# Optimization experiments

Measured on AMD Instinct MI355X. Metric: run time of the kernel, lower is better.

The kernel has to match this reference:

```python
import jax, jax.numpy as jnp
import numpy as np

NEG = -9e15  # sentinel used by the torch module for masked logits


def setup_inputs() -> dict:
    key = jax.random.key(0)
    k_x, k_nl, k_q, k_k, k_v = jax.random.split(key, 5)
    n, m, nhid = 50000, 16, 128
    x = jax.random.normal(k_x, (n, nhid), dtype=jnp.float32)
    neighbor_list = jax.random.randint(k_nl, (n, m), 0, n)  # value n-1 == padding
    # xavier_uniform with gain=1.414 for square (nhid, nhid) matrices
    bound = 1.414 * np.sqrt(6.0 / (nhid + nhid))
    Q = jax.random.uniform(k_q, (nhid, nhid), jnp.float32, -bound, bound)
    K = jax.random.uniform(k_k, (nhid, nhid), jnp.float32, -bound, bound)
    V = jax.random.uniform(k_v, (nhid, nhid), jnp.float32, -bound, bound)
    return {"x": x, "neighbor_list": neighbor_list, "Q": Q, "K": K, "V": V}


def _forward(x, neighbor_list, Q, K, V):
    n, nhid = x.shape
    scare = jnp.asarray(nhid ** 0.5, x.dtype)
    # masks: neighbor index n-1 means padding
    mask = (neighbor_list != n - 1).astype(x.dtype)            # (n, m)
    mask1 = mask[:, :, None] * mask[:, None, :]                # (n, m, m)
    mask2 = jnp.concatenate([jnp.ones((n, 1), x.dtype), mask], axis=1)[:, None, :]  # (n,1,m+1)

    # ---- stage 1: neighbor-level attention ----
    nm = x[neighbor_list]                                      # (n, m, h) gather
    Qn = jnp.einsum('nmk,kh->nmh', nm, Q)
    Kn = jnp.einsum('nmk,kh->nmh', nm, K)
    Vn = jnp.einsum('nmk,kh->nmh', nm, V)
    s = jnp.einsum('nih,njh->nij', Qn, Kn)                     # (n, m, m)
    s = jax.nn.leaky_relu(s, 0.01)
    s = jnp.where(mask1 > 0, s, NEG) * scare                   # faithful: scale after mask
    a = jax.nn.softmax(s, axis=2)                              # dropout is identity (eval)
    nres = jnp.einsum('nij,njh->nih', a, Vn)                   # (n, m, h)

    # ---- stage 2: node-level attention over [self, neighbors] ----
    xr = x[:, None, :]                                         # (n, 1, h)
    cat = jnp.concatenate([xr, nres], axis=1)                  # (n, m+1, h)
    Qx = jnp.einsum('nik,kh->nih', xr, Q)                      # (n, 1, h)
    Kc = jnp.einsum('njk,kh->njh', cat, K)
    Vc = jnp.einsum('njk,kh->njh', cat, V)
    s2 = jnp.einsum('nih,njh->nij', Qx, Kc) * scare            # (n, 1, m+1)
    s2 = jax.nn.leaky_relu(s2, 0.01)
    s2 = jnp.where(mask2 > 0, s2, NEG)
    a2 = jax.nn.softmax(s2, axis=2)
    out = jnp.einsum('nij,njh->nih', a2, Vc)[:, 0, :]          # (n, h)

    # F.normalize: L2 along dim 1, eps 1e-12
    norm = jnp.linalg.norm(out, axis=1, keepdims=True)
    return out / jnp.maximum(norm, 1e-12)


def reference(x, neighbor_list, Q, K, V):
    return _forward(x, neighbor_list, Q, K, V)
```

## Files before the change

### kernel.cpp

```cpp
#include <hip/hip_runtime.h>
#include <math.h>

#define NEG_CONST (-9000000000000000.0f)
#define SCARE 11.313708498984761f

#define DPP_XOR1  0xB1
#define DPP_XOR2  0x4E
#define DPP_XOR7  0x141
#define DPP_XOR15 0x140

template<int CTRL>
__device__ __forceinline__ float dpp_add(float x) {
    int yi = __builtin_amdgcn_update_dpp(0, __float_as_int(x), CTRL, 0xF, 0xF, true);
    return x + __int_as_float(yi);
}
template<int CTRL>
__device__ __forceinline__ float dpp_max(float x) {
    int yi = __builtin_amdgcn_update_dpp(0, __float_as_int(x), CTRL, 0xF, 0xF, true);
    return fmaxf(x, __int_as_float(yi));
}

__device__ __forceinline__ void wave_lds_fence() {
    __builtin_amdgcn_wave_barrier();
    asm volatile("s_waitcnt lgkmcnt(0)" ::: "memory");
    __builtin_amdgcn_wave_barrier();
}
__device__ __forceinline__ void wave_vm_fence() {
    __builtin_amdgcn_wave_barrier();
    asm volatile("s_waitcnt vmcnt(0) lgkmcnt(0)" ::: "memory");
    __builtin_amdgcn_wave_barrier();
}

__global__ __launch_bounds__(256) void small_mm_a(const float* __restrict__ Q,
                                                  const float* __restrict__ K,
                                                  const float* __restrict__ V,
                                                  float* __restrict__ QKt,
                                                  float* __restrict__ VV) {
    int r  = blockIdx.x * 8 + (threadIdx.x >> 5);
    int c0 = (threadIdx.x & 31) * 4;
    float a0 = 0.f, a1 = 0.f, a2 = 0.f, a3 = 0.f;
    if (blockIdx.y == 0) {
        for (int k = 0; k < 128; k += 4) {
            float4 q  = *reinterpret_cast<const float4*>(&Q[r * 128 + k]);
            float4 k0 = *reinterpret_cast<const float4*>(&K[(c0 + 0) * 128 + k]);
            float4 k1 = *reinterpret_cast<const float4*>(&K[(c0 + 1) * 128 + k]);
            float4 k2 = *reinterpret_cast<const float4*>(&K[(c0 + 2) * 128 + k]);
            float4 k3 = *reinterpret_cast<const float4*>(&K[(c0 + 3) * 128 + k]);
            a0 += q.x*k0.x + q.y*k0.y + q.z*k0.z + q.w*k0.w;
            a1 += q.x*k1.x + q.y*k1.y + q.z*k1.z + q.w*k1.w;
            a2 += q.x*k2.x + q.y*k2.y + q.z*k2.z + q.w*k2.w;
            a3 += q.x*k3.x + q.y*k3.y + q.z*k3.z + q.w*k3.w;
        }
        float4 o = {a0, a1, a2, a3};
        *reinterpret_cast<float4*>(&QKt[r * 128 + c0]) = o;
    } else {
        for (int k = 0; k < 128; ++k) {
            float a = V[r * 128 + k];
            float4 b = *reinterpret_cast<const float4*>(&V[k * 128 + c0]);
            a0 += a * b.x; a1 += a * b.y; a2 += a * b.z; a3 += a * b.w;
        }
        float4 o = {a0, a1, a2, a3};
        *reinterpret_cast<float4*>(&VV[r * 128 + c0]) = o;
    }
}

__global__ __launch_bounds__(256) void small_mm_b(const float* __restrict__ QKt,
                                                  const float* __restrict__ V,
                                                  float* __restrict__ MT) {
    int r  = blockIdx.x * 8 + (threadIdx.x >> 5);
    int c0 = (threadIdx.x & 31) * 4;
    float a0 = 0.f, a1 = 0.f, a2 = 0.f, a3 = 0.f;
    for (int k = 0; k < 128; k += 4) {
        float4 q  = *reinterpret_cast<const float4*>(&QKt[r * 128 + k]);
        float4 k0 = *reinterpret_cast<const float4*>(&V[(c0 + 0) * 128 + k]);
        float4 k1 = *reinterpret_cast<const float4*>(&V[(c0 + 1) * 128 + k]);
        float4 k2 = *reinterpret_cast<const float4*>(&V[(c0 + 2) * 128 + k]);
        float4 k3 = *reinterpret_cast<const float4*>(&V[(c0 + 3) * 128 + k]);
        a0 += q.x*k0.x + q.y*k0.y + q.z*k0.z + q.w*k0.w;
        a1 += q.x*k1.x + q.y*k1.y + q.z*k1.z + q.w*k1.w;
        a2 += q.x*k2.x + q.y*k2.y + q.z*k2.z + q.w*k2.w;
        a3 += q.x*k3.x + q.y*k3.y + q.z*k3.z + q.w*k3.w;
    }
    float4 o = {a0, a1, a2, a3};
    *reinterpret_cast<float4*>(&MT[r * 128 + c0]) = o;
}

__global__ __launch_bounds__(256) void proj_gemm(
    const float* __restrict__ x,
    const float* __restrict__ W0, const float* __restrict__ W1,
    const float* __restrict__ W2,
    float* __restrict__ G, float* __restrict__ O1, float* __restrict__ O2,
    int n)
{
    __shared__ __align__(16) float xs[32][132];
    __shared__ __align__(16) float ws[32][132];

    const float* Wsel[3] = {W0, W1, W2};
    float*       Osel[3] = {G, O1, O2};
    const int    osr[3]  = {256, 128, 128};
    const int    oof[3]  = {128, 0, 0};
    int yb = blockIdx.y;
    const float* W = Wsel[yb];
    float*       O = Osel[yb];
    int ostride = osr[yb];
    int ooff = oof[yb];
    int row0 = blockIdx.x * 128;
    int tid = threadIdx.x;
    int tr = tid >> 4, tc = tid & 15;

    float acc[8][8] = {};
    for (int kk = 0; kk < 128; kk += 32) {
        #pragma unroll
        for (int it = 0; it < 4; ++it) {
            int id = tid + it * 256;
            int r = id >> 3;
            int f = id & 7;
            int grow = row0 + r;
            float4 v = (grow < n)
                ? *reinterpret_cast<const float4*>(&x[(size_t)grow * 128 + kk + f * 4])
                : make_float4(0.f, 0.f, 0.f, 0.f);
            xs[f * 4 + 0][r] = v.x; xs[f * 4 + 1][r] = v.y;
            xs[f * 4 + 2][r] = v.z; xs[f * 4 + 3][r] = v.w;
            if (yb == 0 && grow < n)
                *reinterpret_cast<float4*>(&G[(size_t)grow * 256 + kk + f * 4]) = v;
        }
        #pragma unroll
        for (int it = 0; it < 4; ++it) {
            int id = tid + it * 256;
            int k = id >> 5;
            int c4 = id & 31;
            *reinterpret_cast<float4*>(&ws[k][c4 * 4]) =
                *reinterpret_cast<const float4*>(&W[(size_t)(kk + k) * 128 + c4 * 4]);
        }
        __syncthreads();
        #pragma unroll 4
        for (int k = 0; k < 32; ++k) {
            float4 a0 = *reinterpret_cast<const float4*>(&xs[k][tr * 8]);
            float4 a1 = *reinterpret_cast<const float4*>(&xs[k][tr * 8 + 4]);
            float4 b0 = *reinterpret_cast<const float4*>(&ws[k][tc * 8]);
            float4 b1 = *reinterpret_cast<const float4*>(&ws[k][tc * 8 + 4]);
            float av[8] = {a0.x, a0.y, a0.z, a0.w, a1.x, a1.y, a1.z, a1.w};
            float bv[8] = {b0.x, b0.y, b0.z, b0.w, b1.x, b1.y, b1.z, b1.w};
            #pragma unroll
            for (int i2 = 0; i2 < 8; ++i2)
                #pragma unroll
                for (int j2 = 0; j2 < 8; ++j2)
                    acc[i2][j2] += av[i2] * bv[j2];
        }
        __syncthreads();
    }
    #pragma unroll
    for (int i2 = 0; i2 < 8; ++i2) {
        int grow = row0 + tr * 8 + i2;
        if (grow < n) {
            float4 o0 = {acc[i2][0], acc[i2][1], acc[i2][2], acc[i2][3]};
            float4 o1 = {acc[i2][4], acc[i2][5], acc[i2][6], acc[i2][7]};
            *reinterpret_cast<float4*>(&O[(size_t)grow * ostride + ooff + tc * 8])     = o0;
            *reinterpret_cast<float4*>(&O[(size_t)grow * ostride + ooff + tc * 8 + 4]) = o1;
        }
    }
}

__global__ __launch_bounds__(64, 5) void node_attn(
    const int* __restrict__ nlist,
    const float* __restrict__ G,
    float* uy,
    float* __restrict__ c0a,
    int n)
{
    __shared__ __align__(16) float Bs[2048];
    __shared__ __align__(16) float Ts[16];

    const int l  = threadIdx.x;
    const int g  = l >> 2;
    const int jj = l & 3;
    const int i  = blockIdx.x;

    int nlv = 0;
    if (l < 16) nlv = nlist[(size_t)i * 16 + l];
    unsigned long long mb = __ballot(l < 16 ? (nlv != n - 1) : 0);

    {
        int sub   = l & 31;
        int sigma = ((sub & 3) << 3) | (sub >> 2);
        int half  = l >> 5;
        #pragma unroll
        for (int p = 0; p < 8; ++p) {
            int nr = __shfl(nlv, 2 * p + half, 64);
            const float* src = &G[(size_t)nr * 256 + sigma * 4];
            __builtin_amdgcn_global_load_lds(
                (const __attribute__((address_space(1))) unsigned int*)src,
                (__attribute__((address_space(3))) unsigned int*)&Bs[p * 256],
                16, 0, 0);
        }
    }

    float2 qa = *reinterpret_cast<const float2*>(&G[(size_t)i * 256 + 128 + l * 2]);
    float2 xa = *reinterpret_cast<const float2*>(&G[(size_t)i * 256 + l * 2]);
    float s200 = qa.x * xa.x + qa.y * xa.y;
    s200 = dpp_add<DPP_XOR1>(s200);
    s200 = dpp_add<DPP_XOR2>(s200);
    s200 = dpp_add<DPP_XOR7>(s200);
    s200 = dpp_add<DPP_XOR15>(s200);
    s200 += __shfl_xor(s200, 16, 64);
    s200 += __shfl_xor(s200, 32, 64);

    int nl_g = __shfl(nlv, g, 64);
    float4 A[8];
    {
        const float* ab = &G[(size_t)nl_g * 256 + 128 + jj * 32];
        #pragma unroll
        for (int k4 = 0; k4 < 8; ++k4)
            A[k4] = *reinterpret_cast<const float4*>(&ab[k4 * 4]);
    }

    wave_vm_fence();

    float a[16];
    {
        float sc[16];
        #pragma unroll
        for (int c = 0; c < 16; ++c) {
            const float* bb = &Bs[c * 128 + jj * 4];
            float acc = 0.f;
            #pragma unroll
            for (int k4 = 0; k4 < 8; ++k4) {
                float4 b = *reinterpret_cast<const float4*>(&bb[k4 * 16]);
                acc += A[k4].x * b.x + A[k4].y * b.y + A[k4].z * b.z + A[k4].w * b.w;
            }
            acc = dpp_add<DPP_XOR1>(acc);
            acc = dpp_add<DPP_XOR2>(acc);
            sc[c] = acc;
        }
        bool rlive = (mb >> g) & 1ULL;
        float m = -3.0e38f;
        #pragma unroll
        for (int c = 0; c < 16; ++c) {
            float s = sc[c];
            float slr = s > 0.f ? s : 0.01f * s;
            bool live = rlive && ((mb >> c) & 1ULL);
            float sm = (live ? slr : NEG_CONST) * SCARE;
            sc[c] = sm;
            m = fmaxf(m, sm);
        }
        float ssum = 0.f;
        #pragma unroll
        for (int c = 0; c < 16; ++c) { float p = __expf(sc[c] - m); a[c] = p; ssum += p; }
        float rs = 1.f / ssum;
        #pragma unroll
        for (int c = 0; c < 16; ++c) a[c] *= rs;
    }

    {
        float acc = 0.f;
        #pragma unroll
        for (int k4 = 0; k4 < 8; ++k4) {
            int kx = (k4 + g) & 7;
            float4 b  = *reinterpret_cast<const float4*>(&Bs[g * 128 + kx * 16 + jj * 4]);
            float4 uu = *reinterpret_cast<const float4*>(&uy[(size_t)i * 128 + jj * 32 + kx * 4]);
            acc += uu.x * b.x + uu.y * b.y + uu.z * b.z + uu.w * b.w;
        }
        acc = dpp_add<DPP_XOR1>(acc);
        acc = dpp_add<DPP_XOR2>(acc);
        if (jj == 0) Ts[g] = acc;
    }
    wave_lds_fence();
    float tarr[16];
    {
        #pragma unroll
        for (int q4 = 0; q4 < 4; ++q4) {
            float4 t4 = *reinterpret_cast<const float4*>(&Ts[q4 * 4]);
            tarr[q4 * 4 + 0] = t4.x; tarr[q4 * 4 + 1] = t4.y;
            tarr[q4 * 4 + 2] = t4.z; tarr[q4 * 4 + 3] = t4.w;
        }
    }

    float lg = 0.f;
    #pragma unroll
    for (int k = 0; k < 16; ++k) lg += a[k] * tarr[k];
    {
        float v = lg * SCARE;
        v = v > 0.f ? v : 0.01f * v;
        lg = ((mb >> g) & 1ULL) ? v : NEG_CONST;
    }
    float v0 = s200 * SCARE;
    v0 = v0 > 0.f ? v0 : 0.01f * v0;

    float m17 = lg;
    m17 = dpp_max<DPP_XOR7>(m17);
    m17 = dpp_max<DPP_XOR15>(m17);
    m17 = fmaxf(m17, __shfl_xor(m17, 16, 64));
    m17 = fmaxf(m17, __shfl_xor(m17, 32, 64));
    m17 = fmaxf(m17, v0);
    float pg = __expf(lg - m17);
    float sg = pg;
    sg = dpp_add<DPP_XOR7>(sg);
    sg = dpp_add<DPP_XOR15>(sg);
    sg += __shfl_xor(sg, 16, 64);
    sg += __shfl_xor(sg, 32, 64);
    float p0 = __expf(v0 - m17);
    float inv = 1.f / (sg + p0);
    float a2g = pg * inv;
    float a20 = p0 * inv;

    float w[16];
    #pragma unroll
    for (int k = 0; k < 16; ++k) {
        float wv = a2g * a[k];
        wv = dpp_add<DPP_XOR7>(wv);
        wv = dpp_add<DPP_XOR15>(wv);
        wv += __shfl_xor(wv, 16, 64);
        wv += __shfl_xor(wv, 32, 64);
        w[k] = wv;
    }

    {
        int sg2 = l >> 1;
        int tau = ((sg2 & 7) << 2) | (sg2 >> 3);
        int off2 = (2 * l) & 3;
        float y0 = 0.f, y1 = 0.f;
        #pragma unroll
        for (int k = 0; k < 16; ++k) {
            float2 bp = *reinterpret_cast<const float2*>(&Bs[k * 128 + tau * 4 + off2]);
            y0 += w[k] * bp.x;
            y1 += w[k] * bp.y;
        }
        float2 yw = {y0, y1};
        *reinterpret_cast<float2*>(&uy[(size_t)i * 128 + 2 * l]) = yw;
    }
    if (l == 0) c0a[i] = a20;
}

__global__ __launch_bounds__(256) void ep_gemm(
    const float* __restrict__ y, const float* __restrict__ xV,
    const float* __restrict__ c0a, const float* __restrict__ VVm,
    float* __restrict__ outp, int n)
{
    __shared__ __align__(16) float ysd[32][132];
    __shared__ __align__(16) float wsd[32][132];

    int row0 = blockIdx.x * 128;
    int tid = threadIdx.x;
    int tr = tid >> 4, tc = tid & 15;

    float acc[8][8] = {};
    for (int kk = 0; kk < 128; kk += 32) {
        #pragma unroll
        for (int it = 0; it < 4; ++it) {
            int id = tid + it * 256;
            int r = id >> 3;
            int f = id & 7;
            int grow = row0 + r;
            float4 v = (grow < n)
                ? *reinterpret_cast<const float4*>(&y[(size_t)grow * 128 + kk + f * 4])
                : make_float4(0.f, 0.f, 0.f, 0.f);
            ysd[f * 4 + 0][r] = v.x; ysd[f * 4 + 1][r] = v.y;
            ysd[f * 4 + 2][r] = v.z; ysd[f * 4 + 3][r] = v.w;
        }
        #pragma unroll
        for (int it = 0; it < 4; ++it) {
            int id = tid + it * 256;
            int k = id >> 5;
            int c4 = id & 31;
            *reinterpret_cast<float4*>(&wsd[k][c4 * 4]) =
                *reinterpret_cast<const float4*>(&VVm[(size_t)(kk + k) * 128 + c4 * 4]);
        }
        __syncthreads();
        #pragma unroll 4
        for (int k = 0; k < 32; ++k) {
            float4 a0 = *reinterpret_cast<const float4*>(&ysd[k][tr * 8]);
            float4 a1 = *reinterpret_cast<const float4*>(&ysd[k][tr * 8 + 4]);
            float4 b0 = *reinterpret_cast<const float4*>(&wsd[k][tc * 8]);
            float4 b1 = *reinterpret_cast<const float4*>(&wsd[k][tc * 8 + 4]);
            float av[8] = {a0.x, a0.y, a0.z, a0.w, a1.x, a1.y, a1.z, a1.w};
            float bv[8] = {b0.x, b0.y, b0.z, b0.w, b1.x, b1.y, b1.z, b1.w};
            #pragma unroll
            for (int i2 = 0; i2 < 8; ++i2)
                #pragma unroll
                for (int j2 = 0; j2 < 8; ++j2)
                    acc[i2][j2] += av[i2] * bv[j2];
        }
        __syncthreads();
    }

    #pragma unroll
    for (int i2 = 0; i2 < 8; ++i2) {
        int grow = row0 + tr * 8 + i2;
        float c0v = 0.f;
        float4 xv0 = make_float4(0.f, 0.f, 0.f, 0.f);
        float4 xv1 = make_float4(0.f, 0.f, 0.f, 0.f);
        if (grow < n) {
            c0v = c0a[grow];
            xv0 = *reinterpret_cast<const float4*>(&xV[(size_t)grow * 128 + tc * 8]);
            xv1 = *reinterpret_cast<const float4*>(&xV[(size_t)grow * 128 + tc * 8 + 4]);
        }
        float o[8];
        o[0] = acc[i2][0] + c0v * xv0.x; o[1] = acc[i2][1] + c0v * xv0.y;
        o[2] = acc[i2][2] + c0v * xv0.z; o[3] = acc[i2][3] + c0v * xv0.w;
        o[4] = acc[i2][4] + c0v * xv1.x; o[5] = acc[i2][5] + c0v * xv1.y;
        o[6] = acc[i2][6] + c0v * xv1.z; o[7] = acc[i2][7] + c0v * xv1.w;
        float ss = 0.f;
        #pragma unroll
        for (int j2 = 0; j2 < 8; ++j2) ss += o[j2] * o[j2];
        ss = dpp_add<DPP_XOR1>(ss);
        ss = dpp_add<DPP_XOR2>(ss);
        ss = dpp_add<DPP_XOR7>(ss);
        ss = dpp_add<DPP_XOR15>(ss);
        float d = fmaxf(sqrtf(ss), 1e-12f);
        float rd = 1.f / d;
        if (grow < n) {
            float4 o0 = {o[0] * rd, o[1] * rd, o[2] * rd, o[3] * rd};
            float4 o1 = {o[4] * rd, o[5] * rd, o[6] * rd, o[7] * rd};
            *reinterpret_cast<float4*>(&outp[(size_t)grow * 128 + tc * 8])     = o0;
            *reinterpret_cast<float4*>(&outp[(size_t)grow * 128 + tc * 8 + 4]) = o1;
        }
    }
}

extern "C" void kernel_launch(void* const* d_in, const int* in_sizes, int n_in,
                              void* d_out, int out_size, void* d_ws, size_t ws_size,
                              hipStream_t stream) {
    const float* x     = (const float*)d_in[0];
    const int*   nlist = (const int*)d_in[1];
    const float* Q     = (const float*)d_in[2];
    const float* K     = (const float*)d_in[3];
    const float* V     = (const float*)d_in[4];
    float* out = (float*)d_out;
    int n = in_sizes[0] / 128;

    float* ws   = (float*)d_ws;
    float* QKt  = ws;
    float* MT   = ws + 16384;
    float* VV   = ws + 32768;
    float* c0a  = ws + 49152;
    float* G    = c0a + n;
    float* uarr = G + (size_t)n * 256;
    float* xV   = uarr + (size_t)n * 128;

    small_mm_a<<<dim3(16, 2), 256, 0, stream>>>(Q, K, V, QKt, VV);
    small_mm_b<<<dim3(16), 256, 0, stream>>>(QKt, V, MT);
    dim3 g2((n + 127) / 128, 3);
    proj_gemm<<<g2, 256, 0, stream>>>(x, QKt, MT, V, G, uarr, xV, n);
    node_attn<<<n, 64, 0, stream>>>(nlist, G, uarr, c0a, n);
    ep_gemm<<<(n + 127) / 128, 256, 0, stream>>>(uarr, xV, c0a, VV, out, n);
}
```

Before: 299.1 us.

## Drop xV projection and VV precompute by applying V twice in epilogue

Removes the third projection output (x·V) and the V·V precompute. The epilogue now forms y·V + c0·x (read from the x columns of G) and multiplies by V again in a second in-block GEMM, staging the first result through shared memory. This avoids writing and re-reading an n×128 intermediate and one projection pass. In exchange the epilogue does twice the FLOPs plus extra shared-memory transposes and barriers.

```diff
diff --git a/kernel.cpp b/kernel.cpp
--- a/kernel.cpp
+++ b/kernel.cpp
@@ -31,37 +31,25 @@
     __builtin_amdgcn_wave_barrier();
 }
 
-__global__ __launch_bounds__(256) void small_mm_a(const float* __restrict__ Q,
-                                                  const float* __restrict__ K,
-                                                  const float* __restrict__ V,
-                                                  float* __restrict__ QKt,
-                                                  float* __restrict__ VV) {
+__global__ __launch_bounds__(256) void small_mm_qkt(const float* __restrict__ Q,
+                                                    const float* __restrict__ K,
+                                                    float* __restrict__ QKt) {
     int r  = blockIdx.x * 8 + (threadIdx.x >> 5);
     int c0 = (threadIdx.x & 31) * 4;
     float a0 = 0.f, a1 = 0.f, a2 = 0.f, a3 = 0.f;
-    if (blockIdx.y == 0) {
-        for (int k = 0; k < 128; k += 4) {
-            float4 q  = *reinterpret_cast<const float4*>(&Q[r * 128 + k]);
-            float4 k0 = *reinterpret_cast<const float4*>(&K[(c0 + 0) * 128 + k]);
-            float4 k1 = *reinterpret_cast<const float4*>(&K[(c0 + 1) * 128 + k]);
-            float4 k2 = *reinterpret_cast<const float4*>(&K[(c0 + 2) * 128 + k]);
-            float4 k3 = *reinterpret_cast<const float4*>(&K[(c0 + 3) * 128 + k]);
-            a0 += q.x*k0.x + q.y*k0.y + q.z*k0.z + q.w*k0.w;
-            a1 += q.x*k1.x + q.y*k1.y + q.z*k1.z + q.w*k1.w;
-            a2 += q.x*k2.x + q.y*k2.y + q.z*k2.z + q.w*k2.w;
-            a3 += q.x*k3.x + q.y*k3.y + q.z*k3.z + q.w*k3.w;
-        }
-        float4 o = {a0, a1, a2, a3};
-        *reinterpret_cast<float4*>(&QKt[r * 128 + c0]) = o;
-    } else {
-        for (int k = 0; k < 128; ++k) {
-            float a = V[r * 128 + k];
-            float4 b = *reinterpret_cast<const float4*>(&V[k * 128 + c0]);
-            a0 += a * b.x; a1 += a * b.y; a2 += a * b.z; a3 += a * b.w;
-        }
-        float4 o = {a0, a1, a2, a3};
-        *reinterpret_cast<float4*>(&VV[r * 128 + c0]) = o;
-    }
+    for (int k = 0; k < 128; k += 4) {
+        float4 q  = *reinterpret_cast<const float4*>(&Q[r * 128 + k]);
+        float4 k0 = *reinterpret_cast<const float4*>(&K[(c0 + 0) * 128 + k]);
+        float4 k1 = *reinterpret_cast<const float4*>(&K[(c0 + 1) * 128 + k]);
+        float4 k2 = *reinterpret_cast<const float4*>(&K[(c0 + 2) * 128 + k]);
+        float4 k3 = *reinterpret_cast<const float4*>(&K[(c0 + 3) * 128 + k]);
+        a0 += q.x*k0.x + q.y*k0.y + q.z*k0.z + q.w*k0.w;
+        a1 += q.x*k1.x + q.y*k1.y + q.z*k1.z + q.w*k1.w;
+        a2 += q.x*k2.x + q.y*k2.y + q.z*k2.z + q.w*k2.w;
+        a3 += q.x*k3.x + q.y*k3.y + q.z*k3.z + q.w*k3.w;
+    }
+    float4 o = {a0, a1, a2, a3};
+    *reinterpret_cast<float4*>(&QKt[r * 128 + c0]) = o;
 }
 
 __global__ __launch_bounds__(256) void small_mm_b(const float* __restrict__ QKt,
@@ -88,22 +76,16 @@
 __global__ __launch_bounds__(256) void proj_gemm(
     const float* __restrict__ x,
     const float* __restrict__ W0, const float* __restrict__ W1,
-    const float* __restrict__ W2,
-    float* __restrict__ G, float* __restrict__ O1, float* __restrict__ O2,
-    int n)
+    float* __restrict__ G, float* __restrict__ O1, int n)
 {
     __shared__ __align__(16) float xs[32][132];
     __shared__ __align__(16) float ws[32][132];
 
-    const float* Wsel[3] = {W0, W1, W2};
-    float*       Osel[3] = {G, O1, O2};
-    const int    osr[3]  = {256, 128, 128};
-    const int    oof[3]  = {128, 0, 0};
     int yb = blockIdx.y;
-    const float* W = Wsel[yb];
-    float*       O = Osel[yb];
-    int ostride = osr[yb];
-    int ooff = oof[yb];
+    const float* W = yb ? W1 : W0;
+    float*       O = yb ? O1 : G;
+    int ostride = yb ? 128 : 256;
+    int ooff    = yb ? 0 : 128;
     int row0 = blockIdx.x * 128;
     int tid = threadIdx.x;
     int tr = tid >> 4, tc = tid & 15;
@@ -331,12 +313,12 @@
     if (l == 0) c0a[i] = a20;
 }
 
-__global__ __launch_bounds__(256) void ep_gemm(
-    const float* __restrict__ y, const float* __restrict__ xV,
-    const float* __restrict__ c0a, const float* __restrict__ VVm,
+__global__ __launch_bounds__(256) void ep_fused(
+    const float* __restrict__ y, const float* __restrict__ G,
+    const float* __restrict__ c0a, const float* __restrict__ Vw,
     float* __restrict__ outp, int n)
 {
-    __shared__ __align__(16) float ysd[32][132];
+    __shared__ __align__(16) float as_[32][132];
     __shared__ __align__(16) float wsd[32][132];
 
     int row0 = blockIdx.x * 128;
@@ -354,8 +336,8 @@
             float4 v = (grow < n)
                 ? *reinterpret_cast<const float4*>(&y[(size_t)grow * 128 + kk + f * 4])
                 : make_float4(0.f, 0.f, 0.f, 0.f);
-            ysd[f * 4 + 0][r] = v.x; ysd[f * 4 + 1][r] = v.y;
-            ysd[f * 4 + 2][r] = v.z; ysd[f * 4 + 3][r] = v.w;
+            as_[f * 4 + 0][r] = v.x; as_[f * 4 + 1][r] = v.y;
+            as_[f * 4 + 2][r] = v.z; as_[f * 4 + 3][r] = v.w;
         }
         #pragma unroll
         for (int it = 0; it < 4; ++it) {
@@ -363,13 +345,13 @@
             int k = id >> 5;
             int c4 = id & 31;
             *reinterpret_cast<float4*>(&wsd[k][c4 * 4]) =
-                *reinterpret_cast<const float4*>(&VVm[(size_t)(kk + k) * 128 + c4 * 4]);
+                *reinterpret_cast<const float4*>(&Vw[(size_t)(kk + k) * 128 + c4 * 4]);
         }
         __syncthreads();
         #pragma unroll 4
         for (int k = 0; k < 32; ++k) {
-            float4 a0 = *reinterpret_cast<const float4*>(&ysd[k][tr * 8]);
-            float4 a1 = *reinterpret_cast<const float4*>(&ysd[k][tr * 8 + 4]);
+            float4 a0 = *reinterpret_cast<const float4*>(&as_[k][tr * 8]);
+            float4 a1 = *reinterpret_cast<const float4*>(&as_[k][tr * 8 + 4]);
             float4 b0 = *reinterpret_cast<const float4*>(&wsd[k][tc * 8]);
             float4 b1 = *reinterpret_cast<const float4*>(&wsd[k][tc * 8 + 4]);
             float av[8] = {a0.x, a0.y, a0.z, a0.w, a1.x, a1.y, a1.z, a1.w};
@@ -386,22 +368,59 @@
     #pragma unroll
     for (int i2 = 0; i2 < 8; ++i2) {
         int grow = row0 + tr * 8 + i2;
-        float c0v = 0.f;
-        float4 xv0 = make_float4(0.f, 0.f, 0.f, 0.f);
-        float4 xv1 = make_float4(0.f, 0.f, 0.f, 0.f);
         if (grow < n) {
-            c0v = c0a[grow];
-            xv0 = *reinterpret_cast<const float4*>(&xV[(size_t)grow * 128 + tc * 8]);
-            xv1 = *reinterpret_cast<const float4*>(&xV[(size_t)grow * 128 + tc * 8 + 4]);
-        }
-        float o[8];
-        o[0] = acc[i2][0] + c0v * xv0.x; o[1] = acc[i2][1] + c0v * xv0.y;
-        o[2] = acc[i2][2] + c0v * xv0.z; o[3] = acc[i2][3] + c0v * xv0.w;
-        o[4] = acc[i2][4] + c0v * xv1.x; o[5] = acc[i2][5] + c0v * xv1.y;
-        o[6] = acc[i2][6] + c0v * xv1.z; o[7] = acc[i2][7] + c0v * xv1.w;
+            float c0v = c0a[grow];
+            float4 g0 = *reinterpret_cast<const float4*>(&G[(size_t)grow * 256 + tc * 8]);
+            float4 g1 = *reinterpret_cast<const float4*>(&G[(size_t)grow * 256 + tc * 8 + 4]);
+            acc[i2][0] += c0v * g0.x; acc[i2][1] += c0v * g0.y;
+            acc[i2][2] += c0v * g0.z; acc[i2][3] += c0v * g0.w;
+            acc[i2][4] += c0v * g1.x; acc[i2][5] += c0v * g1.y;
+            acc[i2][6] += c0v * g1.z; acc[i2][7] += c0v * g1.w;
+        }
+    }
+
+    float acc2[8][8] = {};
+    for (int kk = 0; kk < 128; kk += 32) {
+        __syncthreads();
+        int tcl = tc - (kk >> 3);
+        if (tcl >= 0 && tcl < 4) {
+            #pragma unroll
+            for (int j2 = 0; j2 < 8; ++j2)
+                #pragma unroll
+                for (int i2 = 0; i2 < 8; ++i2)
+                    as_[tcl * 8 + j2][tr * 8 + i2] = acc[i2][j2];
+        }
+        #pragma unroll
+        for (int it = 0; it < 4; ++it) {
+            int id = tid + it * 256;
+            int k = id >> 5;
+            int c4 = id & 31;
+            *reinterpret_cast<float4*>(&wsd[k][c4 * 4]) =
+                *reinterpret_cast<const float4*>(&Vw[(size_t)(kk + k) * 128 + c4 * 4]);
+        }
+        __syncthreads();
+        #pragma unroll 4
+        for (int k = 0; k < 32; ++k) {
+            float4 a0 = *reinterpret_cast<const float4*>(&as_[k][tr * 8]);
+            float4 a1 = *reinterpret_cast<const float4*>(&as_[k][tr * 8 + 4]);
+            float4 b0 = *reinterpret_cast<const float4*>(&wsd[k][tc * 8]);
+            float4 b1 = *reinterpret_cast<const float4*>(&wsd[k][tc * 8 + 4]);
+            float av[8] = {a0.x, a0.y, a0.z, a0.w, a1.x, a1.y, a1.z, a1.w};
+            float bv[8] = {b0.x, b0.y, b0.z, b0.w, b1.x, b1.y, b1.z, b1.w};
+            #pragma unroll
+            for (int i2 = 0; i2 < 8; ++i2)
+                #pragma unroll
+                for (int j2 = 0; j2 < 8; ++j2)
+                    acc2[i2][j2] += av[i2] * bv[j2];
+        }
+    }
+
+    #pragma unroll
+    for (int i2 = 0; i2 < 8; ++i2) {
+        int grow = row0 + tr * 8 + i2;
         float ss = 0.f;
         #pragma unroll
-        for (int j2 = 0; j2 < 8; ++j2) ss += o[j2] * o[j2];
+        for (int j2 = 0; j2 < 8; ++j2) ss += acc2[i2][j2] * acc2[i2][j2];
         ss = dpp_add<DPP_XOR1>(ss);
         ss = dpp_add<DPP_XOR2>(ss);
         ss = dpp_add<DPP_XOR7>(ss);
@@ -409,8 +428,8 @@
         float d = fmaxf(sqrtf(ss), 1e-12f);
         float rd = 1.f / d;
         if (grow < n) {
-            float4 o0 = {o[0] * rd, o[1] * rd, o[2] * rd, o[3] * rd};
-            float4 o1 = {o[4] * rd, o[5] * rd, o[6] * rd, o[7] * rd};
+            float4 o0 = {acc2[i2][0] * rd, acc2[i2][1] * rd, acc2[i2][2] * rd, acc2[i2][3] * rd};
+            float4 o1 = {acc2[i2][4] * rd, acc2[i2][5] * rd, acc2[i2][6] * rd, acc2[i2][7] * rd};
             *reinterpret_cast<float4*>(&outp[(size_t)grow * 128 + tc * 8])     = o0;
             *reinterpret_cast<float4*>(&outp[(size_t)grow * 128 + tc * 8 + 4]) = o1;
         }
@@ -431,16 +450,14 @@
     float* ws   = (float*)d_ws;
     float* QKt  = ws;
     float* MT   = ws + 16384;
-    float* VV   = ws + 32768;
-    float* c0a  = ws + 49152;
+    float* c0a  = ws + 32768;
     float* G    = c0a + n;
     float* uarr = G + (size_t)n * 256;
-    float* xV   = uarr + (size_t)n * 128;
-
-    small_mm_a<<<dim3(16, 2), 256, 0, stream>>>(Q, K, V, QKt, VV);
+
+    small_mm_qkt<<<dim3(16), 256, 0, stream>>>(Q, K, QKt);
     small_mm_b<<<dim3(16), 256, 0, stream>>>(QKt, V, MT);
-    dim3 g2((n + 127) / 128, 3);
-    proj_gemm<<<g2, 256, 0, stream>>>(x, QKt, MT, V, G, uarr, xV, n);
+    dim3 g2((n + 127) / 128, 2);
+    proj_gemm<<<g2, 256, 0, stream>>>(x, QKt, MT, G, uarr, n);
     node_attn<<<n, 64, 0, stream>>>(nlist, G, uarr, c0a, n);
-    ep_gemm<<<(n + 127) / 128, 256, 0, stream>>>(uarr, xV, c0a, VV, out, n);
-}
+    ep_fused<<<(n + 127) / 128, 256, 0, stream>>>(uarr, G, c0a, V, out, n);
+}
```

Result: no change. 303.8 us (+1.6%).
